# Optimization experiments

Measured on AMD Instinct MI355X. Metric: run time of the kernel, lower is better.

Reference implementation:

```python
import jax, jax.numpy as jnp
import numpy as np

NUM_CLS = 80
SR = 0.2
STRIDES = (8, 16, 32, 64, 128)
IMG = 1280
FMAPS = [(IMG // s, IMG // s) for s in STRIDES]
MAX_BOXES = 128
BIG_AREA = 1e7  # padding value for box-area argmin (matches tf.pad constant)


def _shrink_boxes(boxes, fw, fh, stride, sr):
    # shrink gt boxes by `sr` around their center and snap to feature-grid ints
    b = boxes / stride
    cx = (b[:, 0] + b[:, 2]) * 0.5
    cy = (b[:, 1] + b[:, 3]) * 0.5
    hw = (b[:, 2] - b[:, 0]) * sr * 0.5
    hh = (b[:, 3] - b[:, 1]) * sr * 0.5
    px1 = jnp.clip(jnp.floor(cx - hw), 0, fw - 1).astype(jnp.int32)
    py1 = jnp.clip(jnp.floor(cy - hh), 0, fh - 1).astype(jnp.int32)
    px2 = jnp.clip(jnp.ceil(cx + hw).astype(jnp.int32), px1 + 1, fw)
    py2 = jnp.clip(jnp.ceil(cy + hh).astype(jnp.int32), py1 + 1, fh)
    return px1, py1, px2, py2


def _level_targets(boxes, labels, valid, sel_w, fh, fw, stride):
    # Vectorized replacement of the per-box tf.map_fn + tf.pad + argmin + gather_nd.
    # The original builds a padded dense map per box; padding values are:
    #   cls one-hot -> 0, soft weight -> 1, regr mask -> 0, regr target -> 0, area -> 1e7.
    # We instead compute dense [K,fh,fw] maps and mask, which is the same math.
    px1, py1, px2, py2 = _shrink_boxes(boxes, fw, fh, stride, SR)  # [K]
    sx = (jnp.arange(fw, dtype=jnp.float32) + 0.5) * stride  # pixel-center x
    sy = (jnp.arange(fh, dtype=jnp.float32) + 0.5) * stride  # pixel-center y
    dl = jnp.maximum(sx[None, None, :] - boxes[:, 0, None, None], 0.0)  # [K,fh,fw]
    dt = jnp.maximum(sy[None, :, None] - boxes[:, 1, None, None], 0.0)
    dr = jnp.maximum(boxes[:, 2, None, None] - sx[None, None, :], 0.0)
    db = jnp.maximum(boxes[:, 3, None, None] - sy[None, :, None], 0.0)
    gx = jnp.arange(fw)[None, None, :]
    gy = jnp.arange(fh)[None, :, None]
    in_box = ((gx >= px1[:, None, None]) & (gx < px2[:, None, None])
              & (gy >= py1[:, None, None]) & (gy < py2[:, None, None])
              & valid[:, None, None])  # [K,fh,fw] positive region per box
    area = jnp.where(in_box, (dl + dr) * (dt + db), BIG_AREA)
    win = jnp.argmin(area, axis=0)  # [fh,fw] smallest-area box per pixel

    take = lambda a: jnp.take_along_axis(a, win[None], axis=0)[0]
    is_pos = take(in_box).astype(jnp.float32)
    dl_w, dt_w, dr_w, db_w = take(dl), take(dt), take(dr), take(db)

    # anchor-point weight min/max ratio (guard 0/0 which is only hit off-target)
    num = jnp.minimum(dl_w, dr_w) * jnp.minimum(dt_w, db_w)
    den = jnp.maximum(dl_w, dr_w) * jnp.maximum(dt_w, db_w)
    ap = jnp.where(den > 0, num / jnp.maximum(den, 1e-12), 0.0)
    soft = jnp.where(is_pos > 0, ap * sel_w[win], 1.0)

    onehot = jax.nn.one_hot(labels[win], NUM_CLS, dtype=jnp.float32) * is_pos[..., None]
    regr = (jnp.stack([dl_w, dt_w, dr_w, db_w], axis=-1) / (4.0 * stride)) * is_pos[..., None]
    extra = jnp.stack([soft, is_pos], axis=-1)  # [fh,fw,2] soft weight + pos mask
    cls_t = jnp.concatenate([onehot, extra], axis=-1).reshape(fh * fw, NUM_CLS + 2)
    regr_t = jnp.concatenate([regr, extra], axis=-1).reshape(fh * fw, 4 + 2)
    return cls_t, regr_t


def reference(gt_boxes, feature_select_weight, feature_maps_shape):
    # feature_maps_shape is accepted for signature fidelity; shapes must be
    # static under jit so we use the FMAPS constant (same values).
    labels = gt_boxes[:, 4].astype(jnp.int32)
    boxes = gt_boxes[:, :4]
    valid = jnp.any(jnp.abs(boxes) > 0, axis=1)  # trim_zero_padding_boxes as mask
    cls_list, regr_list = [], []
    for lvl, stride in enumerate(STRIDES):
        fh, fw = FMAPS[lvl]
        c, r = _level_targets(boxes, labels, valid,
                              feature_select_weight[:, lvl], fh, fw, stride)
        cls_list.append(c)
        regr_list.append(r)
    return jnp.concatenate(cls_list, axis=0), jnp.concatenate(regr_list, axis=0)


def setup_inputs():
    key = jax.random.key(0)
    k1, k2, k3, k4 = jax.random.split(key, 4)
    xy = jax.random.uniform(k1, (MAX_BOXES, 2), minval=0.0, maxval=IMG - 64.0)
    wh = jax.random.uniform(k2, (MAX_BOXES, 2), minval=32.0, maxval=420.0)
    x2y2 = jnp.minimum(xy + wh, IMG - 1.0)
    labels = jax.random.randint(k3, (MAX_BOXES, 1), 0, NUM_CLS).astype(jnp.float32)
    gt = jnp.concatenate([xy, x2y2, labels], axis=-1)
    # zero out last quarter to exercise the zero-padding trim path
    pad_mask = (jnp.arange(MAX_BOXES) < MAX_BOXES * 3 // 4).astype(jnp.float32)
    gt = gt * pad_mask[:, None]
    fsw = jax.random.uniform(k4, (MAX_BOXES, len(STRIDES)))
    fshape = jnp.array(FMAPS, dtype=jnp.int32)
    return {"gt_boxes": gt, "feature_select_weight": fsw,
            "feature_maps_shape": fshape}
```

## Files before the change

kernel.cpp:

```cpp
#include <hip/hip_runtime.h>
#include <math.h>
#include <limits.h>

#define NUM_CLS   80
#define MAX_BOXES 128
#define NLVL      5
#define BIG_AREA  1.0e7f
#define TOTAL_PIX 34100
#define PPB       128

#define INIT_KEY  0x4B18968000000000ULL

__device__ __forceinline__ int level_base(int lvl) {
    switch (lvl) {
        case 0:  return 0;
        case 1:  return 25600;
        case 2:  return 32000;
        case 3:  return 33600;
        default: return 34000;
    }
}

__global__ __launch_bounds__(256) void init_winner(unsigned long long* __restrict__ w) {
    const int i = blockIdx.x * 256 + threadIdx.x;
    if (i < TOTAL_PIX) w[i] = INIT_KEY;
}

__global__ __launch_bounds__(256) void scatter_kernel(
    const float* __restrict__ gt,
    unsigned long long* __restrict__ w)
{
    const int gtid = blockIdx.x * 256 + threadIdx.x;
    const int pair = gtid >> 6;
    const int lane = threadIdx.x & 63;
    if (pair >= MAX_BOXES * NLVL) return;
    const int box = pair & (MAX_BOXES - 1);
    const int lvl = pair >> 7;

    const float x1 = gt[box * 5 + 0];
    const float y1 = gt[box * 5 + 1];
    const float x2 = gt[box * 5 + 2];
    const float y2 = gt[box * 5 + 3];
    const bool valid = (fabsf(x1) > 0.f) || (fabsf(y1) > 0.f) ||
                       (fabsf(x2) > 0.f) || (fabsf(y2) > 0.f);
    if (!valid) return;

    const float stride = (float)(8 << lvl);
    const float inv_s  = 1.0f / stride;
    const int   fw     = 160 >> lvl;
    const float fwm1   = (float)(fw - 1);

    const float bx1 = x1 * inv_s, by1 = y1 * inv_s;
    const float bx2 = x2 * inv_s, by2 = y2 * inv_s;
    const float cx = (bx1 + bx2) * 0.5f;
    const float cy = (by1 + by2) * 0.5f;
    const float hw = ((bx2 - bx1) * 0.2f) * 0.5f;
    const float hh = ((by2 - by1) * 0.2f) * 0.5f;
    const int px1 = (int)fminf(fmaxf(floorf(cx - hw), 0.f), fwm1);
    const int py1 = (int)fminf(fmaxf(floorf(cy - hh), 0.f), fwm1);
    const int px2 = min(max((int)ceilf(cx + hw), px1 + 1), fw);
    const int py2 = min(max((int)ceilf(cy + hh), py1 + 1), fw);

    const int rw = px2 - px1;
    const int n  = rw * (py2 - py1);
    const int base = level_base(lvl);

    for (int i = lane; i < n; i += 64) {
        const int ry = i / rw;
        const int rx = i - ry * rw;
        const int gx = px1 + rx;
        const int gy = py1 + ry;
        const float sx = ((float)gx + 0.5f) * stride;
        const float sy = ((float)gy + 0.5f) * stride;
        const float dl = fmaxf(sx - x1, 0.f);
        const float dt = fmaxf(sy - y1, 0.f);
        const float dr = fmaxf(x2 - sx, 0.f);
        const float db = fmaxf(y2 - sy, 0.f);
        const float area = (dl + dr) * (dt + db);
        const unsigned long long key =
            ((unsigned long long)__float_as_uint(area) << 32) | (unsigned)box;
        atomicMin(&w[base + gy * fw + gx], key);
    }
}

__global__ __launch_bounds__(256) void gather_kernel(
    const float* __restrict__ gt,
    const float* __restrict__ fsw,
    const unsigned long long* __restrict__ w,
    float* __restrict__ out_cls,
    float* __restrict__ out_reg)
{
    __shared__ float4 sbx[MAX_BOXES];
    __shared__ float  ssw[MAX_BOXES][NLVL];
    __shared__ int    slab[MAX_BOXES];
    __shared__ float  st_soft[PPB];
    __shared__ float  st_ispos[PPB];
    __shared__ int    st_lab[PPB];
    __shared__ float  st_reg[PPB][4];

    const int t = threadIdx.x;
    const int block_base = blockIdx.x * PPB;

    if (t < MAX_BOXES) {
        const float x1 = gt[t * 5 + 0];
        const float y1 = gt[t * 5 + 1];
        const float x2 = gt[t * 5 + 2];
        const float y2 = gt[t * 5 + 3];
        sbx[t]  = make_float4(x1, y1, x2, y2);
        slab[t] = (int)gt[t * 5 + 4];
    } else {
        const int b = t - MAX_BOXES;
        #pragma unroll
        for (int l = 0; l < NLVL; ++l) ssw[b][l] = fsw[b * NLVL + l];
    }
    __syncthreads();

    const int count = min(PPB, TOTAL_PIX - block_base);

    if (t < PPB && t < count) {
        const int pid = block_base + t;
        int lvl, fw, lp; float stride;
        if      (pid < 25600) { lvl = 0; fw = 160; lp = pid;         stride = 8.f;   }
        else if (pid < 32000) { lvl = 1; fw = 80;  lp = pid - 25600; stride = 16.f;  }
        else if (pid < 33600) { lvl = 2; fw = 40;  lp = pid - 32000; stride = 32.f;  }
        else if (pid < 34000) { lvl = 3; fw = 20;  lp = pid - 33600; stride = 64.f;  }
        else                  { lvl = 4; fw = 10;  lp = pid - 34000; stride = 128.f; }
        const int gy = lp / fw;
        const int gx = lp - gy * fw;
        const float sx = ((float)gx + 0.5f) * stride;
        const float sy = ((float)gy + 0.5f) * stride;

        const unsigned long long key = w[pid];
        const bool pos = key < INIT_KEY;
        const int  win = (int)(unsigned)key;

        const float4 b = sbx[win];
        const float dl = fmaxf(sx - b.x, 0.f);
        const float dt = fmaxf(sy - b.y, 0.f);
        const float dr = fmaxf(b.z - sx, 0.f);
        const float db = fmaxf(b.w - sy, 0.f);

        const float is_pos = pos ? 1.0f : 0.0f;
        const float num = fminf(dl, dr) * fminf(dt, db);
        const float den = fmaxf(dl, dr) * fmaxf(dt, db);
        const float ap  = (den > 0.f) ? num / fmaxf(den, 1e-12f) : 0.0f;
        const float soft = pos ? ap * ssw[win][lvl] : 1.0f;

        const float rs = 0.25f / stride;
        st_soft[t]  = soft;
        st_ispos[t] = is_pos;
        st_lab[t]   = slab[win];
        st_reg[t][0] = dl * rs * is_pos;
        st_reg[t][1] = dt * rs * is_pos;
        st_reg[t][2] = dr * rs * is_pos;
        st_reg[t][3] = db * rs * is_pos;
    }
    __syncthreads();

    if (count == PPB) {
        float4* cp = (float4*)(out_cls + (size_t)block_base * (NUM_CLS + 2));
        for (int q = t; q < PPB * (NUM_CLS + 2) / 4; q += 256) {
            const int flat = q * 4;
            const int row0 = (int)((unsigned)flat / 82u);
            const int col0 = flat - row0 * 82;
            float v[4];
            #pragma unroll
            for (int k = 0; k < 4; ++k) {
                int r = row0, c = col0 + k;
                if (c >= 82) { c -= 82; ++r; }
                const float ip = st_ispos[r];
                float val;
                if (c < NUM_CLS)       val = (c == st_lab[r] && ip != 0.f) ? 1.0f : 0.0f;
                else if (c == NUM_CLS) val = st_soft[r];
                else                   val = ip;
                v[k] = val;
            }
            cp[q] = make_float4(v[0], v[1], v[2], v[3]);
        }
        float4* rp = (float4*)(out_reg + (size_t)block_base * 6);
        for (int q = t; q < PPB * 6 / 4; q += 256) {
            const int flat = q * 4;
            const int row0 = (int)((unsigned)flat / 6u);
            const int col0 = flat - row0 * 6;
            float v[4];
            #pragma unroll
            for (int k = 0; k < 4; ++k) {
                int r = row0, c = col0 + k;
                if (c >= 6) { c -= 6; ++r; }
                v[k] = (c < 4) ? st_reg[r][c] : ((c == 4) ? st_soft[r] : st_ispos[r]);
            }
            rp[q] = make_float4(v[0], v[1], v[2], v[3]);
        }
    } else {
        float* cbase = out_cls + (size_t)block_base * (NUM_CLS + 2);
        for (int q = t; q < count * (NUM_CLS + 2); q += 256) {
            const int r = (int)((unsigned)q / 82u);
            const int c = q - r * 82;
            const float ip = st_ispos[r];
            float val;
            if (c < NUM_CLS)       val = (c == st_lab[r] && ip != 0.f) ? 1.0f : 0.0f;
            else if (c == NUM_CLS) val = st_soft[r];
            else                   val = ip;
            cbase[q] = val;
        }
        float* rbase = out_reg + (size_t)block_base * 6;
        for (int q = t; q < count * 6; q += 256) {
            const int r = (int)((unsigned)q / 6u);
            const int c = q - r * 6;
            rbase[q] = (c < 4) ? st_reg[r][c] : ((c == 4) ? st_soft[r] : st_ispos[r]);
        }
    }
}

extern "C" void kernel_launch(void* const* d_in, const int* in_sizes, int n_in,
                              void* d_out, int out_size, void* d_ws, size_t ws_size,
                              hipStream_t stream) {
    (void)in_sizes; (void)n_in; (void)out_size; (void)ws_size;
    const float* gt  = (const float*)d_in[0];
    const float* fsw = (const float*)d_in[1];
    float* out_cls = (float*)d_out;
    float* out_reg = out_cls + (size_t)TOTAL_PIX * (NUM_CLS + 2);
    unsigned long long* w = (unsigned long long*)d_ws;

    init_winner  <<<(TOTAL_PIX + 255) / 256, 256, 0, stream>>>(w);
    scatter_kernel<<<(MAX_BOXES * NLVL * 64 + 255) / 256, 256, 0, stream>>>(gt, w);
    gather_kernel<<<(TOTAL_PIX + PPB - 1) / PPB, 256, 0, stream>>>(gt, fsw, w, out_cls, out_reg);
}
```

Measured before the change: 69.44 us.

## Fuse init/scatter/gather into one kernel with per-block box culling

Replaces the three-kernel pipeline (init winner buffer, atomicMin scatter, gather) with one fused kernel. Each block covers 256 pixels of a single level, culls the boxes whose shrunk rectangle overlaps its rows into shared memory, and has every pixel loop over those candidates to find the minimum-area key. This removes two launches, the global workspace traffic and the 64-bit atomics. In exchange each pixel does a serial loop over up to ~96 candidate boxes, and only 135 blocks are launched.

```diff
diff --git a/kernel.cpp b/kernel.cpp
--- a/kernel.cpp
+++ b/kernel.cpp
@@ -7,99 +7,48 @@
 #define NLVL      5
 #define BIG_AREA  1.0e7f
 #define TOTAL_PIX 34100
-#define PPB       128
+#define PPB       256
+#define NBLK      135
 
 #define INIT_KEY  0x4B18968000000000ULL
 
-__device__ __forceinline__ int level_base(int lvl) {
-    switch (lvl) {
-        case 0:  return 0;
-        case 1:  return 25600;
-        case 2:  return 32000;
-        case 3:  return 33600;
-        default: return 34000;
-    }
-}
-
-__global__ __launch_bounds__(256) void init_winner(unsigned long long* __restrict__ w) {
-    const int i = blockIdx.x * 256 + threadIdx.x;
-    if (i < TOTAL_PIX) w[i] = INIT_KEY;
-}
-
-__global__ __launch_bounds__(256) void scatter_kernel(
-    const float* __restrict__ gt,
-    unsigned long long* __restrict__ w)
-{
-    const int gtid = blockIdx.x * 256 + threadIdx.x;
-    const int pair = gtid >> 6;
-    const int lane = threadIdx.x & 63;
-    if (pair >= MAX_BOXES * NLVL) return;
-    const int box = pair & (MAX_BOXES - 1);
-    const int lvl = pair >> 7;
-
-    const float x1 = gt[box * 5 + 0];
-    const float y1 = gt[box * 5 + 1];
-    const float x2 = gt[box * 5 + 2];
-    const float y2 = gt[box * 5 + 3];
-    const bool valid = (fabsf(x1) > 0.f) || (fabsf(y1) > 0.f) ||
-                       (fabsf(x2) > 0.f) || (fabsf(y2) > 0.f);
-    if (!valid) return;
-
-    const float stride = (float)(8 << lvl);
-    const float inv_s  = 1.0f / stride;
-    const int   fw     = 160 >> lvl;
-    const float fwm1   = (float)(fw - 1);
-
-    const float bx1 = x1 * inv_s, by1 = y1 * inv_s;
-    const float bx2 = x2 * inv_s, by2 = y2 * inv_s;
-    const float cx = (bx1 + bx2) * 0.5f;
-    const float cy = (by1 + by2) * 0.5f;
-    const float hw = ((bx2 - bx1) * 0.2f) * 0.5f;
-    const float hh = ((by2 - by1) * 0.2f) * 0.5f;
-    const int px1 = (int)fminf(fmaxf(floorf(cx - hw), 0.f), fwm1);
-    const int py1 = (int)fminf(fmaxf(floorf(cy - hh), 0.f), fwm1);
-    const int px2 = min(max((int)ceilf(cx + hw), px1 + 1), fw);
-    const int py2 = min(max((int)ceilf(cy + hh), py1 + 1), fw);
-
-    const int rw = px2 - px1;
-    const int n  = rw * (py2 - py1);
-    const int base = level_base(lvl);
-
-    for (int i = lane; i < n; i += 64) {
-        const int ry = i / rw;
-        const int rx = i - ry * rw;
-        const int gx = px1 + rx;
-        const int gy = py1 + ry;
-        const float sx = ((float)gx + 0.5f) * stride;
-        const float sy = ((float)gy + 0.5f) * stride;
-        const float dl = fmaxf(sx - x1, 0.f);
-        const float dt = fmaxf(sy - y1, 0.f);
-        const float dr = fmaxf(x2 - sx, 0.f);
-        const float db = fmaxf(y2 - sy, 0.f);
-        const float area = (dl + dr) * (dt + db);
-        const unsigned long long key =
-            ((unsigned long long)__float_as_uint(area) << 32) | (unsigned)box;
-        atomicMin(&w[base + gy * fw + gx], key);
-    }
-}
-
-__global__ __launch_bounds__(256) void gather_kernel(
+__global__ __launch_bounds__(256) void fcos_targets_fused(
     const float* __restrict__ gt,
     const float* __restrict__ fsw,
-    const unsigned long long* __restrict__ w,
     float* __restrict__ out_cls,
     float* __restrict__ out_reg)
 {
     __shared__ float4 sbx[MAX_BOXES];
-    __shared__ float  ssw[MAX_BOXES][NLVL];
     __shared__ int    slab[MAX_BOXES];
+    __shared__ float  ssw_l[MAX_BOXES];
+    __shared__ int4   crect[MAX_BOXES];
+    __shared__ float4 cbox[MAX_BOXES];
+    __shared__ int    cid[MAX_BOXES];
+    __shared__ int    cnt;
     __shared__ float  st_soft[PPB];
     __shared__ float  st_ispos[PPB];
     __shared__ int    st_lab[PPB];
     __shared__ float  st_reg[PPB][4];
 
-    const int t = threadIdx.x;
-    const int block_base = blockIdx.x * PPB;
+    const int t   = threadIdx.x;
+    const int bid = blockIdx.x;
+
+    int lvl, lp0, lvl_end;
+    if      (bid < 100) { lvl = 0; lp0 = bid * 256;         lvl_end = 25600; }
+    else if (bid < 125) { lvl = 1; lp0 = (bid - 100) * 256; lvl_end =  6400; }
+    else if (bid < 132) { lvl = 2; lp0 = (bid - 125) * 256; lvl_end =  1600; }
+    else if (bid < 134) { lvl = 3; lp0 = (bid - 132) * 256; lvl_end =   400; }
+    else                { lvl = 4; lp0 = 0;                 lvl_end =   100; }
+    const int   fw     = 160 >> lvl;
+    const float stride = (float)(8 << lvl);
+    const int   count  = min(PPB, lvl_end - lp0);
+    const int   gy_lo  = lp0 / fw;
+    const int   gy_hi  = (lp0 + count - 1) / fw;
+    const int   abs0   = lp0 + ((lvl >= 1) ? 25600 : 0) + ((lvl >= 2) ? 6400 : 0)
+                             + ((lvl >= 3) ? 1600 : 0)  + ((lvl >= 4) ? 400 : 0);
+
+    if (t == 0) cnt = 0;
+    __syncthreads();
 
     if (t < MAX_BOXES) {
         const float x1 = gt[t * 5 + 0];
@@ -108,31 +57,61 @@
         const float y2 = gt[t * 5 + 3];
         sbx[t]  = make_float4(x1, y1, x2, y2);
         slab[t] = (int)gt[t * 5 + 4];
+        const bool valid = (fabsf(x1) > 0.f) || (fabsf(y1) > 0.f) ||
+                           (fabsf(x2) > 0.f) || (fabsf(y2) > 0.f);
+        if (valid) {
+            const float inv_s = 1.0f / stride;
+            const float fwm1  = (float)(fw - 1);
+            const float bx1 = x1 * inv_s, by1 = y1 * inv_s;
+            const float bx2 = x2 * inv_s, by2 = y2 * inv_s;
+            const float cx = (bx1 + bx2) * 0.5f;
+            const float cy = (by1 + by2) * 0.5f;
+            const float hw = ((bx2 - bx1) * 0.2f) * 0.5f;
+            const float hh = ((by2 - by1) * 0.2f) * 0.5f;
+            const int px1 = (int)fminf(fmaxf(floorf(cx - hw), 0.f), fwm1);
+            const int py1 = (int)fminf(fmaxf(floorf(cy - hh), 0.f), fwm1);
+            const int px2 = min(max((int)ceilf(cx + hw), px1 + 1), fw);
+            const int py2 = min(max((int)ceilf(cy + hh), py1 + 1), fw);
+            if (py1 <= gy_hi && py2 > gy_lo) {
+                const int k = atomicAdd(&cnt, 1);
+                crect[k] = make_int4(px1, py1, px2, py2);
+                cbox[k]  = make_float4(x1, y1, x2, y2);
+                cid[k]   = t;
+            }
+        }
     } else {
         const int b = t - MAX_BOXES;
-        #pragma unroll
-        for (int l = 0; l < NLVL; ++l) ssw[b][l] = fsw[b * NLVL + l];
+        ssw_l[b] = fsw[b * NLVL + lvl];
+        ssw_l[b + 64] = fsw[(b + 64) * NLVL + lvl];
     }
     __syncthreads();
 
-    const int count = min(PPB, TOTAL_PIX - block_base);
-
-    if (t < PPB && t < count) {
-        const int pid = block_base + t;
-        int lvl, fw, lp; float stride;
-        if      (pid < 25600) { lvl = 0; fw = 160; lp = pid;         stride = 8.f;   }
-        else if (pid < 32000) { lvl = 1; fw = 80;  lp = pid - 25600; stride = 16.f;  }
-        else if (pid < 33600) { lvl = 2; fw = 40;  lp = pid - 32000; stride = 32.f;  }
-        else if (pid < 34000) { lvl = 3; fw = 20;  lp = pid - 33600; stride = 64.f;  }
-        else                  { lvl = 4; fw = 10;  lp = pid - 34000; stride = 128.f; }
+    if (t < count) {
+        const int lp = lp0 + t;
         const int gy = lp / fw;
         const int gx = lp - gy * fw;
         const float sx = ((float)gx + 0.5f) * stride;
         const float sy = ((float)gy + 0.5f) * stride;
 
-        const unsigned long long key = w[pid];
-        const bool pos = key < INIT_KEY;
-        const int  win = (int)(unsigned)key;
+        unsigned long long best = INIT_KEY;
+        const int n = cnt;
+        for (int i = 0; i < n; ++i) {
+            const int4 s = crect[i];
+            if ((gx >= s.x) & (gx < s.z) & (gy >= s.y) & (gy < s.w)) {
+                const float4 b = cbox[i];
+                const float dl = fmaxf(sx - b.x, 0.f);
+                const float dt = fmaxf(sy - b.y, 0.f);
+                const float dr = fmaxf(b.z - sx, 0.f);
+                const float db = fmaxf(b.w - sy, 0.f);
+                const float area = (dl + dr) * (dt + db);
+                const unsigned long long key =
+                    ((unsigned long long)__float_as_uint(area) << 32) | (unsigned)cid[i];
+                best = (key < best) ? key : best;
+            }
+        }
+
+        const bool pos = best < INIT_KEY;
+        const int  win = (int)(unsigned)best;
 
         const float4 b = sbx[win];
         const float dl = fmaxf(sx - b.x, 0.f);
@@ -144,7 +123,7 @@
         const float num = fminf(dl, dr) * fminf(dt, db);
         const float den = fmaxf(dl, dr) * fmaxf(dt, db);
         const float ap  = (den > 0.f) ? num / fmaxf(den, 1e-12f) : 0.0f;
-        const float soft = pos ? ap * ssw[win][lvl] : 1.0f;
+        const float soft = pos ? ap * ssw_l[win] : 1.0f;
 
         const float rs = 0.25f / stride;
         st_soft[t]  = soft;
@@ -158,7 +137,7 @@
     __syncthreads();
 
     if (count == PPB) {
-        float4* cp = (float4*)(out_cls + (size_t)block_base * (NUM_CLS + 2));
+        float4* cp = (float4*)(out_cls + (size_t)abs0 * (NUM_CLS + 2));
         for (int q = t; q < PPB * (NUM_CLS + 2) / 4; q += 256) {
             const int flat = q * 4;
             const int row0 = (int)((unsigned)flat / 82u);
@@ -177,7 +156,7 @@
             }
             cp[q] = make_float4(v[0], v[1], v[2], v[3]);
         }
-        float4* rp = (float4*)(out_reg + (size_t)block_base * 6);
+        float4* rp = (float4*)(out_reg + (size_t)abs0 * 6);
         for (int q = t; q < PPB * 6 / 4; q += 256) {
             const int flat = q * 4;
             const int row0 = (int)((unsigned)flat / 6u);
@@ -192,7 +171,7 @@
             rp[q] = make_float4(v[0], v[1], v[2], v[3]);
         }
     } else {
-        float* cbase = out_cls + (size_t)block_base * (NUM_CLS + 2);
+        float* cbase = out_cls + (size_t)abs0 * (NUM_CLS + 2);
         for (int q = t; q < count * (NUM_CLS + 2); q += 256) {
             const int r = (int)((unsigned)q / 82u);
             const int c = q - r * 82;
@@ -203,7 +182,7 @@
             else                   val = ip;
             cbase[q] = val;
         }
-        float* rbase = out_reg + (size_t)block_base * 6;
+        float* rbase = out_reg + (size_t)abs0 * 6;
         for (int q = t; q < count * 6; q += 256) {
             const int r = (int)((unsigned)q / 6u);
             const int c = q - r * 6;
@@ -215,14 +194,11 @@
 extern "C" void kernel_launch(void* const* d_in, const int* in_sizes, int n_in,
                               void* d_out, int out_size, void* d_ws, size_t ws_size,
                               hipStream_t stream) {
-    (void)in_sizes; (void)n_in; (void)out_size; (void)ws_size;
+    (void)in_sizes; (void)n_in; (void)out_size; (void)d_ws; (void)ws_size;
     const float* gt  = (const float*)d_in[0];
     const float* fsw = (const float*)d_in[1];
     float* out_cls = (float*)d_out;
     float* out_reg = out_cls + (size_t)TOTAL_PIX * (NUM_CLS + 2);
-    unsigned long long* w = (unsigned long long*)d_ws;
-
-    init_winner  <<<(TOTAL_PIX + 255) / 256, 256, 0, stream>>>(w);
-    scatter_kernel<<<(MAX_BOXES * NLVL * 64 + 255) / 256, 256, 0, stream>>>(gt, w);
-    gather_kernel<<<(TOTAL_PIX + PPB - 1) / PPB, 256, 0, stream>>>(gt, fsw, w, out_cls, out_reg);
+
+    fcos_targets_fused<<<NBLK, 256, 0, stream>>>(gt, fsw, out_cls, out_reg);
 }
```

Result: slower. 74.68 us (+7.6%).
